# Kernel tuning notes

Hardware: AMD Instinct MI355X
Metric: run time of the kernel (lower is better)

The kernel has to match this reference:

```python
import jax, jax.numpy as jnp
import numpy as np

RATIO_DENSE = 0.95   # ratio_th[-2] used for dense matching at conv5_2
RATIO_REFINE = 0.9   # ratio_th[k] used by refine_points
EPS = 1e-8
NEIGHBORS = jnp.array([[0, 0], [0, 1], [1, 0], [1, 1]])  # (x, y) offsets


def setup_inputs() -> dict:
    key = jax.random.key(0)
    k1, k2, k3, k4 = jax.random.split(key, 4)
    return {
        'map_A': jax.random.normal(k1, (1, 512, 96, 96), dtype=jnp.float32),
        'map_B': jax.random.normal(k2, (1, 512, 96, 96), dtype=jnp.float32),
        'act_A': jax.random.normal(k3, (1, 512, 192, 192), dtype=jnp.float32),
        'act_B': jax.random.normal(k4, (1, 512, 192, 192), dtype=jnp.float32),
    }


def _mnn_ratio_mask(sim, ratio):
    """Mutual-NN + ratio-test. sim: [N1, N2] cosine similarities.
    Returns nn12 [N1] (best match in B for each A) and boolean mask [N1]."""
    s12, i12 = jax.lax.top_k(sim, 2)            # [N1, 2]
    d12 = 2.0 - 2.0 * s12                       # cosine sim -> squared L2 dist
    r12 = d12[:, 0] / (d12[:, 1] + EPS)
    nn12 = i12[:, 0]
    s21, i21 = jax.lax.top_k(sim.T, 2)          # [N2, 2]
    d21 = 2.0 - 2.0 * s21
    r21 = d21[:, 0] / (d21[:, 1] + EPS)
    nn21 = i21[:, 0]
    ids1 = jnp.arange(sim.shape[0])
    mask = (ids1 == nn21[nn12]) & (r12 <= ratio) & (r21[nn12] <= ratio)
    return nn12, mask


def reference(map_A, map_B, act_A, act_B):
    ch = map_A.shape[1]
    hA, wA = map_A.shape[2], map_A.shape[3]
    hB, wB = map_B.shape[2], map_B.shape[3]

    # ---- dense_feature_matching (padded / masked form) ----
    d1 = map_A.reshape(ch, -1).T               # [N1, ch]
    d1 = d1 / jnp.linalg.norm(d1, axis=1, keepdims=True)
    d2 = map_B.reshape(ch, -1).T               # [N2, ch]
    d2 = d2 / jnp.linalg.norm(d2, axis=1, keepdims=True)
    sim = d1 @ d2.T                            # [N1, N2], the big one
    nn12, valid = _mnn_ratio_mask(sim, RATIO_DENSE)

    idx = jnp.arange(hA * wA)
    yA, xA = jnp.divmod(idx, wA)
    yB, xB = jnp.divmod(nn12, wB)
    border = ((xA == 0) | (xA == wA - 1) | (yA == 0) | (yA == hA - 1) |
              (xB == 0) | (xB == wB - 1) | (yB == 0) | (yB == hB - 1))
    valid = valid & ~border
    # pad invalid points to (0,0) so refine gathers stay in-bounds
    pA = jnp.stack([jnp.where(valid, xA, 0), jnp.where(valid, yA, 0)])  # [2, P]
    pB = jnp.stack([jnp.where(valid, xB, 0), jnp.where(valid, yB, 0)])

    # ---- refine_points (fully vectorized gather-dot-topk over all P points) ----
    dA = act_A[0] / jnp.sqrt(jnp.sum(act_A[0] ** 2, axis=0, keepdims=True))
    dB = act_B[0] / jnp.sqrt(jnp.sum(act_B[0] ** 2, axis=0, keepdims=True))
    pA2 = pA * 2
    pB2 = pB * 2
    P = pA.shape[1]

    gAx = pA2[0][:, None] + NEIGHBORS[:, 0][None, :]   # [P, 4]
    gAy = pA2[1][:, None] + NEIGHBORS[:, 1][None, :]
    gBx = pB2[0][:, None] + NEIGHBORS[:, 0][None, :]
    gBy = pB2[1][:, None] + NEIGHBORS[:, 1][None, :]
    actAg = dA[:, gAy, gAx]                            # [ch, P, 4]
    actBg = dB[:, gBy, gBx]                            # [ch, P, 4]
    scores = jnp.einsum('cpi,cpj->pij', actAg, actBg)  # [P, 4, 4]

    sA, mA = jax.lax.top_k(scores, 2)                  # [P, 4, 2]
    sA = 2.0 - 2.0 * sA
    ratio_A2B = sA[..., 0] / (sA[..., 1] + EPS)        # [P, 4]
    match_A2B = mA[..., 0]
    score_A2B = sA[..., 0]

    sB, mB = jax.lax.top_k(jnp.swapaxes(scores, 1, 2), 2)
    sB = 2.0 - 2.0 * sB
    ratio_B2A = sB[..., 0] / (sB[..., 1] + EPS)
    match_B2A = mB[..., 0]

    ar = jnp.arange(P)
    ind_A = (ar[:, None] * 4 + match_A2B).reshape(-1)  # [P*4]
    ind_B = (ar[:, None] * 4 + match_B2A).reshape(-1)
    ind = jnp.arange(P * 4)
    mask = (jnp.minimum(ratio_A2B, ratio_B2A) < RATIO_REFINE) & \
           (ind_B[ind_A] == ind).reshape(P, 4)

    # drop the two worst (largest-distance) neighbor candidates per point
    score_masked = jnp.where(mask, score_A2B, 5.0)
    _, discard = jax.lax.top_k(score_masked, 2)
    mask = mask.at[ar, discard[:, 0]].set(False)
    mask = mask.at[ar, discard[:, 1]].set(False)
    mask = mask & valid[:, None]

    refined_A = jnp.stack([gAx, gAy])                                   # [2, P, 4]
    rBx = pB2[0][:, None] + NEIGHBORS[:, 0][match_A2B]
    rBy = pB2[1][:, None] + NEIGHBORS[:, 1][match_A2B]
    refined_B = jnp.stack([rBx, rBy])                                   # [2, P, 4]

    return refined_A, refined_B, mask, scores
```

## Files before the change

kernel.cpp:

```cpp
#include <hip/hip_runtime.h>
#include <stdint.h>

#define CH 512
#define W1 96
#define P1 (W1*W1)
#define W2 192
#define P2 (W2*W2)
#define BM 256
#define BN 256
#define NTT 36
#define BK 32
#define NKS (CH/BK)
#define EPSF 1e-8f
#define RDENSE 0.95f
#define RREFINE 0.9f

typedef __attribute__((ext_vector_type(8))) short bf16x8_t;
typedef __attribute__((ext_vector_type(4))) float f32x4_t;

__device__ __forceinline__ unsigned enc_f32(float f){
  unsigned u = __float_as_uint(f);
  return (u & 0x80000000u) ? ~u : (u | 0x80000000u);
}
__device__ __forceinline__ float dec_f32(unsigned e){
  unsigned u = (e & 0x80000000u) ? (e & 0x7FFFFFFFu) : ~e;
  return __uint_as_float(u);
}
__device__ __forceinline__ unsigned long long packVI(float v, int idx){
  return (((unsigned long long)enc_f32(v)) << 32) | (unsigned)(~(unsigned)idx);
}
__device__ __forceinline__ float packedVal(unsigned long long p){ return dec_f32((unsigned)(p >> 32)); }
__device__ __forceinline__ int packedIdx(unsigned long long p){ return (int)(~(unsigned)(p & 0xFFFFFFFFull)); }
__device__ __forceinline__ void merge2(unsigned long long &b, unsigned long long &s, unsigned long long c){
  if (c > b){ s = b; b = c; } else if (c > s){ s = c; }
}

__device__ __forceinline__ unsigned short f2bf(float f){
  unsigned u = __float_as_uint(f);
  unsigned r = (u + 0x7FFFu + ((u >> 16) & 1u)) >> 16;
  return (unsigned short)r;
}

__device__ __forceinline__ void gload16(const void* g, void* l){
  __builtin_amdgcn_global_load_lds(
      (const __attribute__((address_space(1))) unsigned int*)g,
      (__attribute__((address_space(3))) unsigned int*)l, 16, 0, 0);
}

__global__ void desc_norm(const float* __restrict__ mA, const float* __restrict__ mB,
                          float* __restrict__ inv1, float* __restrict__ inv2){
  int p = blockIdx.x * blockDim.x + threadIdx.x;
  const float* m = (p < P1) ? mA : mB;
  float* o = (p < P1) ? inv1 : inv2;
  int pix = (p < P1) ? p : p - P1;
  float s = 0.f;
  for (int c = 0; c < CH; ++c){ float v = m[c*P1 + pix]; s += v*v; }
  o[pix] = 1.0f / sqrtf(s);
}

__global__ void act_norm(const float* __restrict__ aA, const float* __restrict__ aB,
                         float* __restrict__ invA, float* __restrict__ invB){
  int p = blockIdx.x * blockDim.x + threadIdx.x;
  const float* m = (p < P2) ? aA : aB;
  float* o = (p < P2) ? invA : invB;
  int pix = (p < P2) ? p : p - P2;
  float s = 0.f;
  for (int c = 0; c < CH; ++c){ float v = m[(size_t)c*P2 + pix]; s += v*v; }
  o[pix] = 1.0f / sqrtf(s);
}

__global__ __launch_bounds__(256)
void prep_split(const float* __restrict__ src, const float* __restrict__ inv,
                unsigned short* __restrict__ hi, unsigned short* __restrict__ lo){
  __shared__ float tile[64][65];
  const int pixBase = blockIdx.x * 64;
  const int chBase  = blockIdx.y * 64;
  const int t = threadIdx.x;
  #pragma unroll
  for (int rep = 0; rep < 16; ++rep){
    int idx = rep*256 + t;
    int c = idx >> 6, p = idx & 63;
    tile[c][p] = src[(chBase + c)*P1 + pixBase + p];
  }
  __syncthreads();
  const int p = t >> 2, cg = (t & 3) * 16;
  const int pix = pixBase + p;
  const float iv = inv[pix];
  unsigned short hbuf[16], lbuf[16];
  #pragma unroll
  for (int j = 0; j < 16; ++j){
    float v = tile[cg + j][p] * iv;
    unsigned short h = f2bf(v);
    float hv = __uint_as_float((unsigned)h << 16);
    lbuf[j] = f2bf(v - hv);
    hbuf[j] = h;
  }
  const int c0 = chBase + cg;
  const int kb = c0 >> 5;
  const int ck0 = (c0 & 31) >> 3;
  const int sz = (pix >> 1) & 3;
  size_t base = (size_t)kb*(P1*32) + (size_t)pix*32;
  *(uint4*)(hi + base + ((ck0    ^sz)<<3)) = ((const uint4*)hbuf)[0];
  *(uint4*)(hi + base + (((ck0+1)^sz)<<3)) = ((const uint4*)hbuf)[1];
  *(uint4*)(lo + base + ((ck0    ^sz)<<3)) = ((const uint4*)lbuf)[0];
  *(uint4*)(lo + base + (((ck0+1)^sz)<<3)) = ((const uint4*)lbuf)[1];
}

__global__ __launch_bounds__(512, 2)
void sim_mfma(const unsigned short* __restrict__ Ah, const unsigned short* __restrict__ Al,
              const unsigned short* __restrict__ Bh, const unsigned short* __restrict__ Bl,
              unsigned long long* __restrict__ rowCand,
              unsigned long long* __restrict__ colCand){
  __shared__ __align__(16) char lds[131072];

  const int nwg = NTT*NTT;
  int bid = blockIdx.x;
  int swz = (bid & 7) * (nwg >> 3) + (bid >> 3);
  const int rt = swz / NTT, ct = swz % NTT;
  const int rBase = rt * BM, cBase = ct * BN;

  const int t = threadIdx.x;
  const int w = t >> 6, lane = t & 63;
  const int wr = w >> 2, wc = w & 3;
  const int l15 = lane & 15, lj = lane >> 4;

  const int panel = w >> 1, sub = w & 1;
  const unsigned short* pptr = (panel==0)?Ah:(panel==1)?Al:(panel==2)?Bh:Bl;
  const int Base = (panel < 2) ? rBase : cBase;
  const char* gpan = (const char*)pptr + (size_t)Base*64 + sub*8192;
  char* ldsPan0 = lds + panel*16384 + sub*8192;

  int aOff[8], bOff[4];
  #pragma unroll
  for (int mi = 0; mi < 8; ++mi){
    int rA = wr*128 + mi*16 + l15;
    aOff[mi] = rA*64 + ((lj ^ ((rA >> 1) & 3)) << 4);
  }
  #pragma unroll
  for (int ni = 0; ni < 4; ++ni){
    int rB = wc*64 + ni*16 + l15;
    bOff[ni] = rB*64 + ((lj ^ ((rB >> 1) & 3)) << 4);
  }

  f32x4_t acc[8][4];
  #pragma unroll
  for (int i = 0; i < 8; ++i)
    #pragma unroll
    for (int j = 0; j < 4; ++j)
      #pragma unroll
      for (int r = 0; r < 4; ++r) acc[i][j][r] = 0.f;

  #pragma unroll
  for (int i = 0; i < 8; ++i)
    gload16(gpan + i*1024 + lane*16, ldsPan0 + i*1024);
  __syncthreads();

  for (int ks = 0; ks < NKS; ++ks){
    const int cur = ks & 1;
    if (ks + 1 < NKS){
      const char* gb = gpan + (size_t)(ks+1)*(P1*64);
      char* lb = ldsPan0 + (cur^1)*65536;
      #pragma unroll
      for (int i = 0; i < 8; ++i)
        gload16(gb + i*1024 + lane*16, lb + i*1024);
    }
    const char* bp = lds + cur*65536;
    bf16x8_t ahf[8], alf[8];
    #pragma unroll
    for (int mi = 0; mi < 8; ++mi){
      ahf[mi] = *(const bf16x8_t*)(bp + aOff[mi]);
      alf[mi] = *(const bf16x8_t*)(bp + 16384 + aOff[mi]);
    }
    __builtin_amdgcn_s_setprio(1);
    #pragma unroll
    for (int ni = 0; ni < 4; ++ni){
      bf16x8_t bhf = *(const bf16x8_t*)(bp + 32768 + bOff[ni]);
      bf16x8_t blf = *(const bf16x8_t*)(bp + 49152 + bOff[ni]);
      #pragma unroll
      for (int mi = 0; mi < 8; ++mi){
        acc[mi][ni] = __builtin_amdgcn_mfma_f32_16x16x32_bf16(ahf[mi], bhf, acc[mi][ni], 0, 0, 0);
        acc[mi][ni] = __builtin_amdgcn_mfma_f32_16x16x32_bf16(ahf[mi], blf, acc[mi][ni], 0, 0, 0);
        acc[mi][ni] = __builtin_amdgcn_mfma_f32_16x16x32_bf16(alf[mi], bhf, acc[mi][ni], 0, 0, 0);
      }
    }
    __builtin_amdgcn_s_setprio(0);
    __syncthreads();
  }

  unsigned long long (*rowScr)[4][2] = (unsigned long long (*)[4][2])(lds);
  unsigned long long (*colScr)[2][2] = (unsigned long long (*)[2][2])(lds + 16384);

  #pragma unroll
  for (int mi = 0; mi < 8; ++mi){
    #pragma unroll
    for (int reg = 0; reg < 4; ++reg){
      unsigned long long b = 0ull, s = 0ull;
      #pragma unroll
      for (int ni = 0; ni < 4; ++ni){
        int col = cBase + wc*64 + ni*16 + l15;
        merge2(b, s, packVI(acc[mi][ni][reg], col));
      }
      #pragma unroll
      for (int m = 1; m < 16; m <<= 1){
        unsigned long long ob = __shfl_xor(b, m, 64);
        unsigned long long os = __shfl_xor(s, m, 64);
        merge2(b, s, ob); merge2(b, s, os);
      }
      if (l15 == 0){
        int rowLoc = wr*128 + mi*16 + lj*4 + reg;
        rowScr[rowLoc][wc][0] = b; rowScr[rowLoc][wc][1] = s;
      }
    }
  }
  #pragma unroll
  for (int ni = 0; ni < 4; ++ni){
    unsigned long long b = 0ull, s = 0ull;
    #pragma unroll
    for (int mi = 0; mi < 8; ++mi)
      #pragma unroll
      for (int reg = 0; reg < 4; ++reg){
        int row = rBase + wr*128 + mi*16 + lj*4 + reg;
        merge2(b, s, packVI(acc[mi][ni][reg], row));
      }
    #pragma unroll
    for (int m = 16; m < 64; m <<= 1){
      unsigned long long ob = __shfl_xor(b, m, 64);
      unsigned long long os = __shfl_xor(s, m, 64);
      merge2(b, s, ob); merge2(b, s, os);
    }
    if (lj == 0){
      int colLoc = wc*64 + ni*16 + l15;
      colScr[colLoc][wr][0] = b; colScr[colLoc][wr][1] = s;
    }
  }
  __syncthreads();
  if (t < 256){
    unsigned long long b = 0ull, s = 0ull;
    #pragma unroll
    for (int j = 0; j < 4; ++j){ merge2(b, s, rowScr[t][j][0]); merge2(b, s, rowScr[t][j][1]); }
    rowCand[((long long)ct*P1 + rBase + t)*2 + 0] = b;
    rowCand[((long long)ct*P1 + rBase + t)*2 + 1] = s;
  } else {
    int c = t - 256;
    unsigned long long b = 0ull, s = 0ull;
    #pragma unroll
    for (int j = 0; j < 2; ++j){ merge2(b, s, colScr[c][j][0]); merge2(b, s, colScr[c][j][1]); }
    colCand[((long long)rt*P1 + cBase + c)*2 + 0] = b;
    colCand[((long long)rt*P1 + cBase + c)*2 + 1] = s;
  }
}

__global__ void merge_cand(const unsigned long long* __restrict__ cand,
                           unsigned long long* __restrict__ top,
                           unsigned long long* __restrict__ sec){
  int p = blockIdx.x * blockDim.x + threadIdx.x;
  unsigned long long b = 0ull, s = 0ull;
  for (int tile = 0; tile < NTT; ++tile){
    merge2(b, s, cand[((long long)tile*P1 + p)*2 + 0]);
    merge2(b, s, cand[((long long)tile*P1 + p)*2 + 1]);
  }
  top[p] = b; sec[p] = s;
}

__global__ void match_k(const unsigned long long* __restrict__ rowTop,
                        const unsigned long long* __restrict__ rowSec,
                        const unsigned long long* __restrict__ colTop,
                        const unsigned long long* __restrict__ colSec,
                        int4* __restrict__ pts, int* __restrict__ validArr){
  int p = blockIdx.x * blockDim.x + threadIdx.x;
  unsigned long long rT = rowTop[p], rS = rowSec[p];
  float s0 = packedVal(rT), s1 = packedVal(rS);
  int nn12 = packedIdx(rT);
  float r12 = (2.f - 2.f*s0) / (2.f - 2.f*s1 + EPSF);
  unsigned long long cT = colTop[nn12], cS = colSec[nn12];
  int nn21 = packedIdx(cT);
  float r21 = (2.f - 2.f*packedVal(cT)) / (2.f - 2.f*packedVal(cS) + EPSF);
  int xA = p % W1, yA = p / W1, xB = nn12 % W1, yB = nn12 / W1;
  bool border = (xA==0)||(xA==W1-1)||(yA==0)||(yA==W1-1)||
                (xB==0)||(xB==W1-1)||(yB==0)||(yB==W1-1);
  bool valid = (nn21 == p) && (r12 <= RDENSE) && (r21 <= RDENSE) && !border;
  pts[p] = valid ? make_int4(xA,yA,xB,yB) : make_int4(0,0,0,0);
  validArr[p] = valid ? 1 : 0;
}

__global__ __launch_bounds__(256)
void act_transpose(const float* __restrict__ aA, const float* __restrict__ aB,
                   float* __restrict__ tA, float* __restrict__ tB){
  __shared__ float tile[64][65];
  const int pixBase = blockIdx.x * 64;
  const int chBase  = blockIdx.y * 64;
  const float* src = blockIdx.z ? aB : aA;
  float*       dst = blockIdx.z ? tB : tA;
  const int t = threadIdx.x;
  #pragma unroll
  for (int rep = 0; rep < 16; ++rep){
    int idx = rep*256 + t;
    int c = idx >> 6, p = idx & 63;
    tile[c][p] = src[(size_t)(chBase + c)*P2 + pixBase + p];
  }
  __syncthreads();
  const int p = t >> 2, cg = (t & 3) * 16;
  size_t base = (size_t)(pixBase + p)*CH + chBase + cg;
  #pragma unroll
  for (int q = 0; q < 4; ++q){
    float4 v = make_float4(tile[cg+q*4+0][p], tile[cg+q*4+1][p],
                           tile[cg+q*4+2][p], tile[cg+q*4+3][p]);
    *(float4*)(dst + base + q*4) = v;
  }
}

__global__ __launch_bounds__(256)
void refine_t(const float* __restrict__ tA, const float* __restrict__ tB,
              const float* __restrict__ invA, const float* __restrict__ invB,
              const int4* __restrict__ pts, float* __restrict__ scoresOut){
  int p = (blockIdx.x * blockDim.x + threadIdx.x) >> 6;
  int lane = threadIdx.x & 63;
  int4 q = pts[p];
  const int nbx[4] = {0,0,1,1}, nby[4] = {0,1,0,1};
  int offA[4], offB[4];
  #pragma unroll
  for (int i = 0; i < 4; ++i){
    offA[i] = (2*q.y + nby[i])*W2 + 2*q.x + nbx[i];
    offB[i] = (2*q.w + nby[i])*W2 + 2*q.z + nbx[i];
  }
  float a[4][8], b[4][8];
  #pragma unroll
  for (int i = 0; i < 4; ++i){
    const float* pa = tA + (size_t)offA[i]*CH + lane*8;
    *(float4*)&a[i][0] = *(const float4*)pa;
    *(float4*)&a[i][4] = *(const float4*)(pa + 4);
    const float* pb = tB + (size_t)offB[i]*CH + lane*8;
    *(float4*)&b[i][0] = *(const float4*)pb;
    *(float4*)&b[i][4] = *(const float4*)(pb + 4);
  }
  float acc[16] = {};
  #pragma unroll
  for (int ch = 0; ch < 8; ++ch)
    #pragma unroll
    for (int i = 0; i < 4; ++i)
      #pragma unroll
      for (int j = 0; j < 4; ++j)
        acc[i*4+j] = fmaf(a[i][ch], b[j][ch], acc[i*4+j]);
  #pragma unroll
  for (int m = 1; m < 64; m <<= 1)
    #pragma unroll
    for (int u = 0; u < 16; ++u) acc[u] += __shfl_xor(acc[u], m, 64);
  if (lane == 0){
    float sA[4], sB[4];
    #pragma unroll
    for (int i = 0; i < 4; ++i){ sA[i] = invA[offA[i]]; sB[i] = invB[offB[i]]; }
    float4* o = (float4*)(scoresOut + p*16);
    #pragma unroll
    for (int i = 0; i < 4; ++i)
      o[i] = make_float4(acc[i*4+0]*sA[i]*sB[0], acc[i*4+1]*sA[i]*sB[1],
                         acc[i*4+2]*sA[i]*sB[2], acc[i*4+3]*sA[i]*sB[3]);
  }
}

__global__ __launch_bounds__(256)
void refine(const float* __restrict__ actA, const float* __restrict__ actB,
            const float* __restrict__ invA, const float* __restrict__ invB,
            const int4* __restrict__ pts, float* __restrict__ scoresOut){
  int p = (blockIdx.x * blockDim.x + threadIdx.x) >> 6;
  int lane = threadIdx.x & 63;
  int4 q = pts[p];
  const int nbx[4] = {0,0,1,1}, nby[4] = {0,1,0,1};
  int offA[4], offB[4];
  #pragma unroll
  for (int i = 0; i < 4; ++i){
    offA[i] = (2*q.y + nby[i])*W2 + 2*q.x + nbx[i];
    offB[i] = (2*q.w + nby[i])*W2 + 2*q.z + nbx[i];
  }
  float acc[16] = {};
  #pragma unroll
  for (int k = 0; k < 8; ++k){
    int c = lane + 64*k;
    size_t base = (size_t)c * P2;
    float a0 = actA[base+offA[0]], a1 = actA[base+offA[1]],
          a2 = actA[base+offA[2]], a3 = actA[base+offA[3]];
    float b0 = actB[base+offB[0]], b1 = actB[base+offB[1]],
          b2 = actB[base+offB[2]], b3 = actB[base+offB[3]];
    acc[ 0] = fmaf(a0,b0,acc[ 0]); acc[ 1] = fmaf(a0,b1,acc[ 1]);
    acc[ 2] = fmaf(a0,b2,acc[ 2]); acc[ 3] = fmaf(a0,b3,acc[ 3]);
    acc[ 4] = fmaf(a1,b0,acc[ 4]); acc[ 5] = fmaf(a1,b1,acc[ 5]);
    acc[ 6] = fmaf(a1,b2,acc[ 6]); acc[ 7] = fmaf(a1,b3,acc[ 7]);
    acc[ 8] = fmaf(a2,b0,acc[ 8]); acc[ 9] = fmaf(a2,b1,acc[ 9]);
    acc[10] = fmaf(a2,b2,acc[10]); acc[11] = fmaf(a2,b3,acc[11]);
    acc[12] = fmaf(a3,b0,acc[12]); acc[13] = fmaf(a3,b1,acc[13]);
    acc[14] = fmaf(a3,b2,acc[14]); acc[15] = fmaf(a3,b3,acc[15]);
  }
  #pragma unroll
  for (int m = 1; m < 64; m <<= 1)
    #pragma unroll
    for (int u = 0; u < 16; ++u) acc[u] += __shfl_xor(acc[u], m, 64);
  if (lane == 0){
    float sA[4], sB[4];
    #pragma unroll
    for (int i = 0; i < 4; ++i){ sA[i] = invA[offA[i]]; sB[i] = invB[offB[i]]; }
    float4* o = (float4*)(scoresOut + p*16);
    #pragma unroll
    for (int i = 0; i < 4; ++i)
      o[i] = make_float4(acc[i*4+0]*sA[i]*sB[0], acc[i*4+1]*sA[i]*sB[1],
                         acc[i*4+2]*sA[i]*sB[2], acc[i*4+3]*sA[i]*sB[3]);
  }
}

__global__ void final_k(const float* __restrict__ scores, const int4* __restrict__ pts,
                        const int* __restrict__ validArr, float* __restrict__ out){
  int p = blockIdx.x * blockDim.x + threadIdx.x;
  float sc[16];
  #pragma unroll
  for (int u = 0; u < 16; ++u) sc[u] = scores[p*16 + u];

  int matchA[4]; float ratioA[4], scoreA[4];
  #pragma unroll
  for (int i = 0; i < 4; ++i){
    int bi = 0; float bv = sc[i*4];
    #pragma unroll
    for (int j = 1; j < 4; ++j) if (sc[i*4+j] > bv){ bv = sc[i*4+j]; bi = j; }
    float sv = -3.402823466e38f;
    #pragma unroll
    for (int j = 0; j < 4; ++j) if (j != bi && sc[i*4+j] > sv){ sv = sc[i*4+j]; }
    matchA[i] = bi;
    float d0 = 2.f - 2.f*bv, d1 = 2.f - 2.f*sv;
    ratioA[i] = d0 / (d1 + EPSF); scoreA[i] = d0;
  }
  int matchB[4]; float ratioB[4];
  #pragma unroll
  for (int j = 0; j < 4; ++j){
    int bi = 0; float bv = sc[j];
    #pragma unroll
    for (int i = 1; i < 4; ++i) if (sc[i*4+j] > bv){ bv = sc[i*4+j]; bi = i; }
    float sv = -3.402823466e38f;
    #pragma unroll
    for (int i = 0; i < 4; ++i) if (i != bi && sc[i*4+j] > sv){ sv = sc[i*4+j]; }
    matchB[j] = bi;
    float d0 = 2.f - 2.f*bv, d1 = 2.f - 2.f*sv;
    ratioB[j] = d0 / (d1 + EPSF);
  }
  bool m[4];
  #pragma unroll
  for (int i = 0; i < 4; ++i)
    m[i] = (fminf(ratioA[i], ratioB[i]) < RREFINE) && (matchB[matchA[i]] == i);
  float smk[4];
  #pragma unroll
  for (int i = 0; i < 4; ++i) smk[i] = m[i] ? scoreA[i] : 5.0f;
  int d0i = 0; float d0v = smk[0];
  #pragma unroll
  for (int i = 1; i < 4; ++i) if (smk[i] > d0v){ d0v = smk[i]; d0i = i; }
  int d1i = -1; float d1v = -3.402823466e38f;
  #pragma unroll
  for (int i = 0; i < 4; ++i) if (i != d0i && smk[i] > d1v){ d1v = smk[i]; d1i = i; }
  m[d0i] = false; m[d1i] = false;
  bool v = validArr[p] != 0;
  int4 q = pts[p];
  const int nbx[4] = {0,0,1,1}, nby[4] = {0,1,0,1};
  #pragma unroll
  for (int i = 0; i < 4; ++i){
    out[           p*4 + i] = (float)(2*q.x + nbx[i]);
    out[  P1*4   + p*4 + i] = (float)(2*q.y + nby[i]);
    out[2*P1*4   + p*4 + i] = (float)(2*q.z + nbx[matchA[i]]);
    out[3*P1*4   + p*4 + i] = (float)(2*q.w + nby[matchA[i]]);
    out[4*P1*4   + p*4 + i] = (m[i] && v) ? 1.0f : 0.0f;
  }
}

extern "C" void kernel_launch(void* const* d_in, const int* in_sizes, int n_in,
                              void* d_out, int out_size, void* d_ws, size_t ws_size,
                              hipStream_t stream) {
  const float* mapA = (const float*)d_in[0];
  const float* mapB = (const float*)d_in[1];
  const float* actA = (const float*)d_in[2];
  const float* actB = (const float*)d_in[3];
  float* out = (float*)d_out;

  unsigned short* Ah = (unsigned short*)d_ws;
  unsigned short* Al = Ah + (size_t)P1*CH;
  unsigned short* Bh = Al + (size_t)P1*CH;
  unsigned short* Bl = Bh + (size_t)P1*CH;
  unsigned long long* rowCand = (unsigned long long*)(Bl + (size_t)P1*CH);
  unsigned long long* colCand = rowCand + (size_t)NTT*P1*2;
  unsigned long long* rowTop  = colCand + (size_t)NTT*P1*2;
  unsigned long long* rowSec  = rowTop + P1;
  unsigned long long* colTop  = rowSec + P1;
  unsigned long long* colSec  = colTop + P1;
  float* inv1 = (float*)(colSec + P1);
  float* inv2 = inv1 + P1;
  float* invA = inv2 + P1;
  float* invB = invA + P2;
  int4*  pts  = (int4*)(invB + P2);
  int*   validArr = (int*)(pts + P1);
  float* tA = (float*)(validArr + P1);
  float* tB = tA + (size_t)P2*CH;
  size_t needBytes = (size_t)((char*)(tB + (size_t)P2*CH) - (char*)d_ws);
  const bool useT = ws_size >= needBytes;

  float* scoresOut = out + 4*P1*4 + P1*4;

  desc_norm <<<2*P1/256, 256, 0, stream>>>(mapA, mapB, inv1, inv2);
  act_norm  <<<2*P2/256, 256, 0, stream>>>(actA, actB, invA, invB);
  prep_split<<<dim3(P1/64, CH/64), 256, 0, stream>>>(mapA, inv1, Ah, Al);
  prep_split<<<dim3(P1/64, CH/64), 256, 0, stream>>>(mapB, inv2, Bh, Bl);
  sim_mfma  <<<NTT*NTT, 512, 0, stream>>>(Ah, Al, Bh, Bl, rowCand, colCand);
  merge_cand<<<P1/256, 256, 0, stream>>>(rowCand, rowTop, rowSec);
  merge_cand<<<P1/256, 256, 0, stream>>>(colCand, colTop, colSec);
  match_k   <<<P1/256, 256, 0, stream>>>(rowTop, rowSec, colTop, colSec, pts, validArr);
  if (useT){
    act_transpose<<<dim3(P2/64, CH/64, 2), 256, 0, stream>>>(actA, actB, tA, tB);
    refine_t <<<P1*64/256, 256, 0, stream>>>(tA, tB, invA, invB, pts, scoresOut);
  } else {
    refine   <<<P1*64/256, 256, 0, stream>>>(actA, actB, invA, invB, pts, scoresOut);
  }
  final_k   <<<P1/256, 256, 0, stream>>>(scoresOut, pts, validArr, out);
}
```

Before: 1.764 ms.

## Shrink similarity GEMM tiles to 128x128 with 256 threads and interleaved prefetch

Changes the similarity matmul from 256x256 tiles with 512 threads to 128x128 tiles with 256 threads. This halves LDS use and the accumulator registers, and changes the block-to-XCD mapping so each XCD owns a band of column tiles. The next K-slice prefetch is now spread across the MFMA loop with sched barriers, and the s_setprio hints are dropped. Smaller tiles mean more global traffic per FLOP and twice as many candidate partials for merge_cand to reduce, in exchange for more resident waves and better latency hiding.

```diff
diff --git a/kernel.cpp b/kernel.cpp
--- a/kernel.cpp
+++ b/kernel.cpp
@@ -6,9 +6,8 @@
 #define P1 (W1*W1)
 #define W2 192
 #define P2 (W2*W2)
-#define BM 256
-#define BN 256
-#define NTT 36
+#define TILE 128
+#define NT 72
 #define BK 32
 #define NKS (CH/BK)
 #define EPSF 1e-8f
@@ -106,34 +105,33 @@
   *(uint4*)(lo + base + (((ck0+1)^sz)<<3)) = ((const uint4*)lbuf)[1];
 }
 
-__global__ __launch_bounds__(512, 2)
+__global__ __launch_bounds__(256, 2)
 void sim_mfma(const unsigned short* __restrict__ Ah, const unsigned short* __restrict__ Al,
               const unsigned short* __restrict__ Bh, const unsigned short* __restrict__ Bl,
               unsigned long long* __restrict__ rowCand,
               unsigned long long* __restrict__ colCand){
-  __shared__ __align__(16) char lds[131072];
-
-  const int nwg = NTT*NTT;
-  int bid = blockIdx.x;
-  int swz = (bid & 7) * (nwg >> 3) + (bid >> 3);
-  const int rt = swz / NTT, ct = swz % NTT;
-  const int rBase = rt * BM, cBase = ct * BN;
+  __shared__ __align__(16) char lds[65536];
+
+  const int bid = blockIdx.x;
+  const int xcd = bid & 7, local = bid >> 3;
+  const int rt = local / 9;
+  const int ct = xcd * 9 + (local % 9);
+  const int rBase = rt * TILE, cBase = ct * TILE;
 
   const int t = threadIdx.x;
   const int w = t >> 6, lane = t & 63;
-  const int wr = w >> 2, wc = w & 3;
+  const int wr = w >> 1, wc = w & 1;
   const int l15 = lane & 15, lj = lane >> 4;
 
-  const int panel = w >> 1, sub = w & 1;
-  const unsigned short* pptr = (panel==0)?Ah:(panel==1)?Al:(panel==2)?Bh:Bl;
-  const int Base = (panel < 2) ? rBase : cBase;
-  const char* gpan = (const char*)pptr + (size_t)Base*64 + sub*8192;
-  char* ldsPan0 = lds + panel*16384 + sub*8192;
-
-  int aOff[8], bOff[4];
-  #pragma unroll
-  for (int mi = 0; mi < 8; ++mi){
-    int rA = wr*128 + mi*16 + l15;
+  const unsigned short* pptr = (w==0)?Ah:(w==1)?Al:(w==2)?Bh:Bl;
+  const int Base = (w < 2) ? rBase : cBase;
+  const char* gpan = (const char*)pptr + (size_t)Base*64;
+  char* const myLds0 = lds + w*8192;
+
+  int aOff[4], bOff[4];
+  #pragma unroll
+  for (int mi = 0; mi < 4; ++mi){
+    int rA = wr*64 + mi*16 + l15;
     aOff[mi] = rA*64 + ((lj ^ ((rA >> 1) & 3)) << 4);
   }
   #pragma unroll
@@ -142,9 +140,9 @@
     bOff[ni] = rB*64 + ((lj ^ ((rB >> 1) & 3)) << 4);
   }
 
-  f32x4_t acc[8][4];
-  #pragma unroll
-  for (int i = 0; i < 8; ++i)
+  f32x4_t acc[4][4];
+  #pragma unroll
+  for (int i = 0; i < 4; ++i)
     #pragma unroll
     for (int j = 0; j < 4; ++j)
       #pragma unroll
@@ -152,46 +150,49 @@
 
   #pragma unroll
   for (int i = 0; i < 8; ++i)
-    gload16(gpan + i*1024 + lane*16, ldsPan0 + i*1024);
+    gload16(gpan + i*1024 + lane*16, myLds0 + i*1024);
   __syncthreads();
 
   for (int ks = 0; ks < NKS; ++ks){
     const int cur = ks & 1;
-    if (ks + 1 < NKS){
-      const char* gb = gpan + (size_t)(ks+1)*(P1*64);
-      char* lb = ldsPan0 + (cur^1)*65536;
+    const char* bp = lds + cur*32768;
+    char* nb = myLds0 + (cur^1)*32768;
+    const char* gb = gpan + (size_t)(ks+1)*(P1*64);
+    const bool pf = (ks + 1 < NKS);
+
+    bf16x8_t ahf[4], alf[4], bhf[4], blf[4];
+    #pragma unroll
+    for (int mi = 0; mi < 4; ++mi){
+      ahf[mi] = *(const bf16x8_t*)(bp + aOff[mi]);
+      alf[mi] = *(const bf16x8_t*)(bp + 8192 + aOff[mi]);
+    }
+    #pragma unroll
+    for (int ni = 0; ni < 4; ++ni){
+      bhf[ni] = *(const bf16x8_t*)(bp + 16384 + bOff[ni]);
+      blf[ni] = *(const bf16x8_t*)(bp + 24576 + bOff[ni]);
+    }
+    #pragma unroll
+    for (int ni = 0; ni < 4; ++ni){
+      if (pf){
+        gload16(gb + (ni*2+0)*1024 + lane*16, nb + (ni*2+0)*1024);
+        gload16(gb + (ni*2+1)*1024 + lane*16, nb + (ni*2+1)*1024);
+      }
+      __builtin_amdgcn_sched_barrier(0);
       #pragma unroll
-      for (int i = 0; i < 8; ++i)
-        gload16(gb + i*1024 + lane*16, lb + i*1024);
-    }
-    const char* bp = lds + cur*65536;
-    bf16x8_t ahf[8], alf[8];
-    #pragma unroll
-    for (int mi = 0; mi < 8; ++mi){
-      ahf[mi] = *(const bf16x8_t*)(bp + aOff[mi]);
-      alf[mi] = *(const bf16x8_t*)(bp + 16384 + aOff[mi]);
-    }
-    __builtin_amdgcn_s_setprio(1);
-    #pragma unroll
-    for (int ni = 0; ni < 4; ++ni){
-      bf16x8_t bhf = *(const bf16x8_t*)(bp + 32768 + bOff[ni]);
-      bf16x8_t blf = *(const bf16x8_t*)(bp + 49152 + bOff[ni]);
-      #pragma unroll
-      for (int mi = 0; mi < 8; ++mi){
-        acc[mi][ni] = __builtin_amdgcn_mfma_f32_16x16x32_bf16(ahf[mi], bhf, acc[mi][ni], 0, 0, 0);
-        acc[mi][ni] = __builtin_amdgcn_mfma_f32_16x16x32_bf16(ahf[mi], blf, acc[mi][ni], 0, 0, 0);
-        acc[mi][ni] = __builtin_amdgcn_mfma_f32_16x16x32_bf16(alf[mi], bhf, acc[mi][ni], 0, 0, 0);
+      for (int mi = 0; mi < 4; ++mi){
+        acc[mi][ni] = __builtin_amdgcn_mfma_f32_16x16x32_bf16(ahf[mi], bhf[ni], acc[mi][ni], 0, 0, 0);
+        acc[mi][ni] = __builtin_amdgcn_mfma_f32_16x16x32_bf16(ahf[mi], blf[ni], acc[mi][ni], 0, 0, 0);
+        acc[mi][ni] = __builtin_amdgcn_mfma_f32_16x16x32_bf16(alf[mi], bhf[ni], acc[mi][ni], 0, 0, 0);
       }
     }
-    __builtin_amdgcn_s_setprio(0);
     __syncthreads();
   }
 
-  unsigned long long (*rowScr)[4][2] = (unsigned long long (*)[4][2])(lds);
-  unsigned long long (*colScr)[2][2] = (unsigned long long (*)[2][2])(lds + 16384);
-
-  #pragma unroll
-  for (int mi = 0; mi < 8; ++mi){
+  unsigned long long (*rowScr)[2][2] = (unsigned long long (*)[2][2])(lds);
+  unsigned long long (*colScr)[2][2] = (unsigned long long (*)[2][2])(lds + 8192);
+
+  #pragma unroll
+  for (int mi = 0; mi < 4; ++mi){
     #pragma unroll
     for (int reg = 0; reg < 4; ++reg){
       unsigned long long b = 0ull, s = 0ull;
@@ -207,7 +208,7 @@
         merge2(b, s, ob); merge2(b, s, os);
       }
       if (l15 == 0){
-        int rowLoc = wr*128 + mi*16 + lj*4 + reg;
+        int rowLoc = wr*64 + mi*16 + lj*4 + reg;
         rowScr[rowLoc][wc][0] = b; rowScr[rowLoc][wc][1] = s;
       }
     }
@@ -216,10 +217,10 @@
   for (int ni = 0; ni < 4; ++ni){
     unsigned long long b = 0ull, s = 0ull;
     #pragma unroll
-    for (int mi = 0; mi < 8; ++mi)
+    for (int mi = 0; mi < 4; ++mi)
       #pragma unroll
       for (int reg = 0; reg < 4; ++reg){
-        int row = rBase + wr*128 + mi*16 + lj*4 + reg;
+        int row = rBase + wr*64 + mi*16 + lj*4 + reg;
         merge2(b, s, packVI(acc[mi][ni][reg], row));
       }
     #pragma unroll
@@ -234,14 +235,14 @@
     }
   }
   __syncthreads();
-  if (t < 256){
+  if (t < TILE){
     unsigned long long b = 0ull, s = 0ull;
     #pragma unroll
-    for (int j = 0; j < 4; ++j){ merge2(b, s, rowScr[t][j][0]); merge2(b, s, rowScr[t][j][1]); }
+    for (int j = 0; j < 2; ++j){ merge2(b, s, rowScr[t][j][0]); merge2(b, s, rowScr[t][j][1]); }
     rowCand[((long long)ct*P1 + rBase + t)*2 + 0] = b;
     rowCand[((long long)ct*P1 + rBase + t)*2 + 1] = s;
   } else {
-    int c = t - 256;
+    int c = t - TILE;
     unsigned long long b = 0ull, s = 0ull;
     #pragma unroll
     for (int j = 0; j < 2; ++j){ merge2(b, s, colScr[c][j][0]); merge2(b, s, colScr[c][j][1]); }
@@ -255,7 +256,7 @@
                            unsigned long long* __restrict__ sec){
   int p = blockIdx.x * blockDim.x + threadIdx.x;
   unsigned long long b = 0ull, s = 0ull;
-  for (int tile = 0; tile < NTT; ++tile){
+  for (int tile = 0; tile < NT; ++tile){
     merge2(b, s, cand[((long long)tile*P1 + p)*2 + 0]);
     merge2(b, s, cand[((long long)tile*P1 + p)*2 + 1]);
   }
@@ -479,8 +480,8 @@
   unsigned short* Bh = Al + (size_t)P1*CH;
   unsigned short* Bl = Bh + (size_t)P1*CH;
   unsigned long long* rowCand = (unsigned long long*)(Bl + (size_t)P1*CH);
-  unsigned long long* colCand = rowCand + (size_t)NTT*P1*2;
-  unsigned long long* rowTop  = colCand + (size_t)NTT*P1*2;
+  unsigned long long* colCand = rowCand + (size_t)NT*P1*2;
+  unsigned long long* rowTop  = colCand + (size_t)NT*P1*2;
   unsigned long long* rowSec  = rowTop + P1;
   unsigned long long* colTop  = rowSec + P1;
   unsigned long long* colSec  = colTop + P1;
@@ -501,7 +502,7 @@
   act_norm  <<<2*P2/256, 256, 0, stream>>>(actA, actB, invA, invB);
   prep_split<<<dim3(P1/64, CH/64), 256, 0, stream>>>(mapA, inv1, Ah, Al);
   prep_split<<<dim3(P1/64, CH/64), 256, 0, stream>>>(mapB, inv2, Bh, Bl);
-  sim_mfma  <<<NTT*NTT, 512, 0, stream>>>(Ah, Al, Bh, Bl, rowCand, colCand);
+  sim_mfma  <<<NT*NT, 256, 0, stream>>>(Ah, Al, Bh, Bl, rowCand, colCand);
   merge_cand<<<P1/256, 256, 0, stream>>>(rowCand, rowTop, rowSec);
   merge_cand<<<P1/256, 256, 0, stream>>>(colCand, colTop, colSec);
   match_k   <<<P1/256, 256, 0, stream>>>(rowTop, rowSec, colTop, colSec, pts, validArr);
```

New measurement: 1.669 ms. 5.3% less time.
